# Performance work log

Hardware: AMD Instinct MI355X
Metric: run time of the kernel (lower is better)

Reference implementation:

```python
import jax, jax.numpy as jnp
import numpy as np

M, N, K, D_IN, BATCH = 800, 8, 25, 784, 256
MN = M * N


def _uniform(key, shape, fan_in):
    bound = 1.0 / np.sqrt(fan_in)
    return jax.random.uniform(key, shape, jnp.float32, -bound, bound)


def setup_inputs() -> dict:
    key = jax.random.key(0)
    ks = jax.random.split(key, 7)
    return {
        "batch_x": jax.random.normal(ks[0], (BATCH, D_IN), jnp.float32),
        "W_a": _uniform(ks[1], (M, D_IN), D_IN),   # linear_a: D_in -> m
        "b_a": _uniform(ks[2], (M,), D_IN),
        "W_b": _uniform(ks[3], (MN, MN), MN),      # linear_b: mn -> mn (dominant GEMV)
        "b_b": _uniform(ks[4], (MN,), MN),
        "W_d": _uniform(ks[5], (D_IN, M), M),      # linear_d: m -> D_in
        "b_d": _uniform(ks[6], (D_IN,), M),
    }


def reference(batch_x, W_a, b_a, W_b, b_b, W_d, b_d):
    def step(carry, x):
        x_b, phi = carry
        a = W_a @ x + b_a                                   # (M,)
        # torch: linear_a(x).repeat(1, n) -> TILED layout [g0..g_{M-1}] * N
        sigma = jnp.tile(a, N) + W_b @ x_b + b_b            # (MN,)
        pi = (1.0 - phi) * (sigma - sigma.min() + 1.0)      # (MN,)
        # torch topk(pi, 1, dim=1) on shape (1, MN): single GLOBAL argmax one-hot
        m_pi = jnp.zeros(MN, sigma.dtype).at[jnp.argmax(pi)].set(1.0)
        lam = pi.reshape(M, N).max(axis=1)                  # group max, (M,)
        _, idx = jax.lax.top_k(lam, K)
        m_lam = jnp.zeros(M, sigma.dtype).at[idx].set(1.0)  # k winning groups
        y = jnp.tanh(m_pi * jnp.tile(m_lam, N) * sigma)     # (MN,)
        x_a_pred = W_d @ y.reshape(M, N).max(axis=1) + b_d  # (D_IN,)
        # torch takes max against zero buffers self.phi/self.psi -> max(0, y)
        phi_new = jnp.maximum(0.0, y)
        psi_new = jnp.maximum(0.0, y)
        alpha = psi_new.sum()
        alpha = jnp.where(alpha == 0, jnp.asarray(1.0, alpha.dtype), alpha)
        x_b_new = jax.lax.stop_gradient(psi_new / alpha)
        return (x_b_new, phi_new), (x_a_pred, psi_new)

    init = (jnp.zeros(MN, batch_x.dtype), jnp.zeros(MN, batch_x.dtype))
    (x_b, phi), (preds, psis) = jax.lax.scan(step, init, batch_x)
    return preds, x_b, phi, psis[-1]
```

## Files before the change

kernel.cpp:

```cpp
#include <hip/hip_runtime.h>
#include <math.h>

#define MM     800
#define NN     8
#define KSEL   25
#define DIN    784
#define TSTEPS 256
#define MN     6400
#define SCTH   512
#define NWAVE  8
#define REM    288

#define NEGINF __int_as_float(0xff800000)

typedef float vf4 __attribute__((ext_vector_type(4)));

#define LDS_BARRIER() asm volatile("s_waitcnt lgkmcnt(0)\n\ts_barrier" ::: "memory")

#define WRED_STAGE(ctrl, rm)                                                   \
  {                                                                            \
    const float _ov = __int_as_float(__builtin_amdgcn_update_dpp(              \
        (int)0xFF7FFFFF, __float_as_int(bv), ctrl, rm, 0xF, false));           \
    const int _oi = __builtin_amdgcn_update_dpp(MN, bi, ctrl, rm, 0xF, false); \
    const float _om = __int_as_float(__builtin_amdgcn_update_dpp(              \
        0x7F7FFFFF, __float_as_int(lmin), ctrl, rm, 0xF, false));              \
    lmin = fminf(lmin, _om);                                                   \
    if (_ov > bv || (_ov == bv && _oi < bi)) { bv = _ov; bi = _oi; }           \
  }

#define SEL2(vA, iA, vB, iB)                                                   \
  if ((vB) > (vA)) { (vA) = (vB); (iA) = (iB); }

#define CMB(va, ia, vb, ib)                                                    \
  if ((vb) > (va) || ((vb) == (va) && (ib) < (ia))) { (va) = (vb); (ia) = (ib); }

__global__ __launch_bounds__(256) void gemm_a_kernel(
    const float* __restrict__ x,
    const float* __restrict__ Wa,
    const float* __restrict__ ba,
    float* __restrict__ A)
{
  __shared__ float4 sx4[DIN / 4];
  const int t = blockIdx.x;
  const int tid = threadIdx.x;
  if (tid < DIN / 4) sx4[tid] = ((const float4*)(x + t * DIN))[tid];
  __syncthreads();
  const int lane = tid & 63, wid = tid >> 6;
  for (int m = wid; m < MM; m += 4) {
    const float4* wrow = (const float4*)(Wa + m * DIN);
    float p = 0.f;
    for (int k4 = lane; k4 < DIN / 4; k4 += 64) {
      float4 w = wrow[k4];
      float4 xv = sx4[k4];
      p += w.x * xv.x + w.y * xv.y + w.z * xv.z + w.w * xv.w;
    }
    for (int off = 32; off; off >>= 1) p += __shfl_down(p, off, 64);
    if (lane == 0) A[t * MM + m] = p + ba[m];
  }
}

__global__ __launch_bounds__(256) void transpose_wd(
    const float* __restrict__ Wd, float* __restrict__ WdT)
{
  __shared__ float tile[32][33];
  const int bx = blockIdx.x * 32;
  const int by = blockIdx.y * 32;
  const int tx = threadIdx.x, ty = threadIdx.y;
  for (int r = ty; r < 32; r += 8) {
    int d = by + r, g = bx + tx;
    if (d < DIN && g < MM) tile[r][tx] = Wd[d * MM + g];
  }
  __syncthreads();
  for (int r = ty; r < 32; r += 8) {
    int g = bx + r, d = by + tx;
    if (g < MM && d < DIN) WdT[g * DIN + d] = tile[tx][r];
  }
}

__global__ __launch_bounds__(256) void transpose_wb64(
    const float* __restrict__ Wb, float* __restrict__ WbT)
{
  __shared__ float tile[64][65];
  const int bx = blockIdx.x * 64;
  const int by = blockIdx.y * 64;
  const int tx = threadIdx.x & 15;
  const int ty = threadIdx.x >> 4;
#pragma unroll
  for (int r = 0; r < 64; r += 16) {
    vf4 v = __builtin_nontemporal_load(
        (const vf4*)(Wb + (size_t)(by + r + ty) * MN + bx + 4 * tx));
    tile[r + ty][4 * tx + 0] = v[0];
    tile[r + ty][4 * tx + 1] = v[1];
    tile[r + ty][4 * tx + 2] = v[2];
    tile[r + ty][4 * tx + 3] = v[3];
  }
  __syncthreads();
#pragma unroll
  for (int r = 0; r < 64; r += 16) {
    float4 v;
    v.x = tile[4 * tx + 0][r + ty];
    v.y = tile[4 * tx + 1][r + ty];
    v.z = tile[4 * tx + 2][r + ty];
    v.w = tile[4 * tx + 3][r + ty];
    *(float4*)(WbT + (size_t)(bx + r + ty) * MN + by + 4 * tx) = v;
  }
}

__global__ __launch_bounds__(SCTH) void scan_kernel(
    const float* __restrict__ Wb,
    const float* __restrict__ WbT,
    const float* __restrict__ bb,
    const float* __restrict__ bd,
    const float* __restrict__ Wd,
    const float* __restrict__ WdT,
    const float* __restrict__ A,
    float* __restrict__ out)
{
  __shared__ float s_lam[2][MM];
  __shared__ __align__(16) float s_pmin[2][NWAVE];
  __shared__ __align__(16) float s_pbv[2][NWAVE];
  __shared__ __align__(16) int   s_pbi[2][NWAVE];
  __shared__ __align__(8)  float s_jpi[2][2];

  const int tid = threadIdx.x;
  const int lane = tid & 63, wid = tid >> 6;
  const bool has2 = (tid < REM);
  const int g0 = tid, g1 = tid + SCTH;

  int aoff[2];
  float4 bbv[2][2], av[2][2], cv[2][2];
#pragma unroll
  for (int s = 0; s < 2; s++) {
    const int g = tid + SCTH * s;
    const bool v = (s == 0) || has2;
    aoff[s] = 2 * (g % 100);
    if (v) {
      bbv[s][0] = ((const float4*)bb)[2 * g];
      bbv[s][1] = ((const float4*)bb)[2 * g + 1];
      av[s][0] = ((const float4*)A)[aoff[s]];
      av[s][1] = ((const float4*)A)[aoff[s] + 1];
    } else {
      bbv[s][0] = bbv[s][1] = make_float4(0.f, 0.f, 0.f, 0.f);
      av[s][0] = av[s][1] = make_float4(0.f, 0.f, 0.f, 0.f);
    }
    cv[s][0] = cv[s][1] = make_float4(0.f, 0.f, 0.f, 0.f);
  }
  float4 bd4 = make_float4(0.f, 0.f, 0.f, 0.f);
  if (tid < DIN / 4) bd4 = ((const float4*)bd)[tid];

  int jp = -1;
  float phiv = 0.f;
  int act = 0;

  for (int t = 0; t < TSTEPS; t++) {
    const int p = t & 1;
    const int jpg = jp >> 3;
    const int kxe = jp & 7;

    float4 an[2][2];
#pragma unroll
    for (int s = 0; s < 2; s++) an[s][0] = an[s][1] = make_float4(0.f, 0.f, 0.f, 0.f);
    if (t + 1 < TSTEPS) {
      const float4* ar = (const float4*)(A + (size_t)(t + 1) * MM);
#pragma unroll
      for (int s = 0; s < 2; s++) {
        const bool v = (s == 0) || has2;
        if (v) { an[s][0] = ar[aoff[s]]; an[s][1] = ar[aoff[s] + 1]; }
      }
    }

    float e0[8], e1[8];
    if (act) {
      e0[0] = (av[0][0].x + cv[0][0].x) + bbv[0][0].x;
      e0[1] = (av[0][0].y + cv[0][0].y) + bbv[0][0].y;
      e0[2] = (av[0][0].z + cv[0][0].z) + bbv[0][0].z;
      e0[3] = (av[0][0].w + cv[0][0].w) + bbv[0][0].w;
      e0[4] = (av[0][1].x + cv[0][1].x) + bbv[0][1].x;
      e0[5] = (av[0][1].y + cv[0][1].y) + bbv[0][1].y;
      e0[6] = (av[0][1].z + cv[0][1].z) + bbv[0][1].z;
      e0[7] = (av[0][1].w + cv[0][1].w) + bbv[0][1].w;
      e1[0] = (av[1][0].x + cv[1][0].x) + bbv[1][0].x;
      e1[1] = (av[1][0].y + cv[1][0].y) + bbv[1][0].y;
      e1[2] = (av[1][0].z + cv[1][0].z) + bbv[1][0].z;
      e1[3] = (av[1][0].w + cv[1][0].w) + bbv[1][0].w;
      e1[4] = (av[1][1].x + cv[1][1].x) + bbv[1][1].x;
      e1[5] = (av[1][1].y + cv[1][1].y) + bbv[1][1].y;
      e1[6] = (av[1][1].z + cv[1][1].z) + bbv[1][1].z;
      e1[7] = (av[1][1].w + cv[1][1].w) + bbv[1][1].w;
    } else {
      e0[0] = av[0][0].x + bbv[0][0].x;  e0[1] = av[0][0].y + bbv[0][0].y;
      e0[2] = av[0][0].z + bbv[0][0].z;  e0[3] = av[0][0].w + bbv[0][0].w;
      e0[4] = av[0][1].x + bbv[0][1].x;  e0[5] = av[0][1].y + bbv[0][1].y;
      e0[6] = av[0][1].z + bbv[0][1].z;  e0[7] = av[0][1].w + bbv[0][1].w;
      e1[0] = av[1][0].x + bbv[1][0].x;  e1[1] = av[1][0].y + bbv[1][0].y;
      e1[2] = av[1][0].z + bbv[1][0].z;  e1[3] = av[1][0].w + bbv[1][0].w;
      e1[4] = av[1][1].x + bbv[1][1].x;  e1[5] = av[1][1].y + bbv[1][1].y;
      e1[6] = av[1][1].z + bbv[1][1].z;  e1[7] = av[1][1].w + bbv[1][1].w;
    }

    const int kx0 = (jpg == g0) ? kxe : 8;
    const int kx1 = (has2 && jpg == g1) ? kxe : 8;
    float w0 = (kx0 == 0) ? NEGINF : e0[0];  int x0 = 8 * g0 + 0;
    float w1 = (kx0 == 1) ? NEGINF : e0[1];  int x1 = 8 * g0 + 1;
    float w2 = (kx0 == 2) ? NEGINF : e0[2];  int x2 = 8 * g0 + 2;
    float w3 = (kx0 == 3) ? NEGINF : e0[3];  int x3 = 8 * g0 + 3;
    float w4 = (kx0 == 4) ? NEGINF : e0[4];  int x4 = 8 * g0 + 4;
    float w5 = (kx0 == 5) ? NEGINF : e0[5];  int x5 = 8 * g0 + 5;
    float w6 = (kx0 == 6) ? NEGINF : e0[6];  int x6 = 8 * g0 + 6;
    float w7 = (kx0 == 7) ? NEGINF : e0[7];  int x7 = 8 * g0 + 7;
    SEL2(w0, x0, w1, x1); SEL2(w2, x2, w3, x3);
    SEL2(w4, x4, w5, x5); SEL2(w6, x6, w7, x7);
    SEL2(w0, x0, w2, x2); SEL2(w4, x4, w6, x6);
    SEL2(w0, x0, w4, x4);
    const float mxg0 = w0;
    float y0 = (has2 && kx1 != 0) ? e1[0] : NEGINF;  int z0 = has2 ? 8 * g1 + 0 : MN;
    float y1 = (has2 && kx1 != 1) ? e1[1] : NEGINF;  int z1 = has2 ? 8 * g1 + 1 : MN;
    float y2 = (has2 && kx1 != 2) ? e1[2] : NEGINF;  int z2 = has2 ? 8 * g1 + 2 : MN;
    float y3 = (has2 && kx1 != 3) ? e1[3] : NEGINF;  int z3 = has2 ? 8 * g1 + 3 : MN;
    float y4 = (has2 && kx1 != 4) ? e1[4] : NEGINF;  int z4 = has2 ? 8 * g1 + 4 : MN;
    float y5 = (has2 && kx1 != 5) ? e1[5] : NEGINF;  int z5 = has2 ? 8 * g1 + 5 : MN;
    float y6 = (has2 && kx1 != 6) ? e1[6] : NEGINF;  int z6 = has2 ? 8 * g1 + 6 : MN;
    float y7 = (has2 && kx1 != 7) ? e1[7] : NEGINF;  int z7 = has2 ? 8 * g1 + 7 : MN;
    SEL2(y0, z0, y1, z1); SEL2(y2, z2, y3, z3);
    SEL2(y4, z4, y5, z5); SEL2(y6, z6, y7, z7);
    SEL2(y0, z0, y2, z2); SEL2(y4, z4, y6, z6);
    SEL2(y0, z0, y4, z4);
    const float mxg1 = y0;
    float bv = w0; int bi = x0;
    SEL2(bv, bi, y0, z0);

    float gm0, gm1;
    {
      float a = fmaxf(e0[0], e0[1]), b = fmaxf(e0[2], e0[3]);
      float c = fmaxf(e0[4], e0[5]), d = fmaxf(e0[6], e0[7]);
      gm0 = fmaxf(fmaxf(a, b), fmaxf(c, d));
      a = fmaxf(e1[0], e1[1]); b = fmaxf(e1[2], e1[3]);
      c = fmaxf(e1[4], e1[5]); d = fmaxf(e1[6], e1[7]);
      gm1 = fmaxf(fmaxf(a, b), fmaxf(c, d));
    }
    float lmin;
    {
      float a = fminf(e0[0], e0[1]), b = fminf(e0[2], e0[3]);
      float c = fminf(e0[4], e0[5]), d = fminf(e0[6], e0[7]);
      float m0 = fminf(fminf(a, b), fminf(c, d));
      a = fminf(e1[0], e1[1]); b = fminf(e1[2], e1[3]);
      c = fminf(e1[4], e1[5]); d = fminf(e1[6], e1[7]);
      float m1 = fminf(fminf(a, b), fminf(c, d));
      lmin = has2 ? fminf(m0, m1) : m0;
    }
    s_lam[p][g0] = gm0;
    if (has2) s_lam[p][g1] = gm1;

    if (jpg == g0 || (has2 && jpg == g1)) {
      const bool own0 = (jpg == g0);
      float sjp = own0 ? e0[0] : e1[0];
#pragma unroll
      for (int k = 1; k < 8; k++) {
        const float cand = own0 ? e0[k] : e1[k];
        sjp = (kxe == k) ? cand : sjp;
      }
      s_jpi[p][0] = own0 ? mxg0 : mxg1;
      s_jpi[p][1] = sjp;
    }

    WRED_STAGE(0x111, 0xF);
    WRED_STAGE(0x112, 0xF);
    WRED_STAGE(0x114, 0xF);
    WRED_STAGE(0x118, 0xF);
    WRED_STAGE(0x142, 0xa);
    WRED_STAGE(0x143, 0xc);
    if (lane == 63) {
      s_pmin[p][wid] = lmin;
      s_pbv[p][wid] = bv;
      s_pbi[p][wid] = bi;
    }

    LDS_BARRIER();

    const float4 qa = ((const float4*)&s_pmin[p][0])[0];
    const float4 qb = ((const float4*)&s_pmin[p][0])[1];
    const float4 ra = ((const float4*)&s_pbv[p][0])[0];
    const float4 rb = ((const float4*)&s_pbv[p][0])[1];
    const int4  ua = ((const int4*)&s_pbi[p][0])[0];
    const int4  ub = ((const int4*)&s_pbi[p][0])[1];
    const float2 jpi = *(const float2*)&s_jpi[p][0];

    float smin, sigj;
    int jstar;
    {
      const float mn = fminf(fminf(fminf(qa.x, qa.y), fminf(qa.z, qa.w)),
                             fminf(fminf(qb.x, qb.y), fminf(qb.z, qb.w)));
      float V0 = ra.x, V1 = ra.y, V2 = ra.z, V3 = ra.w;
      float V4 = rb.x, V5 = rb.y, V6 = rb.z, V7 = rb.w;
      int I0 = ua.x, I1 = ua.y, I2 = ua.z, I3 = ua.w;
      int I4 = ub.x, I5 = ub.y, I6 = ub.z, I7 = ub.w;
      CMB(V0, I0, V1, I1); CMB(V2, I2, V3, I3);
      CMB(V4, I4, V5, I5); CMB(V6, I6, V7, I7);
      CMB(V0, I0, V2, I2); CMB(V4, I4, V6, I6);
      CMB(V0, I0, V4, I4);
      int js = I0;
      float sv = V0;
      if (jp >= 0) {
        const float sjp = jpi.y;
        const float piA = V0 - mn + 1.f;
        const float pip = (sjp - mn + 1.f) * (1.f - phiv);
        if (pip > piA || (pip == piA && jp < I0)) { js = jp; sv = sjp; }
      }
      smin = mn;
      jstar = js;
      sigj = sv;
    }
    const int jsr = __builtin_amdgcn_readfirstlane(jstar);
    const int gw = jsr >> 3;
    const int q = jsr % MM;

    float4 wd4 = make_float4(0.f, 0.f, 0.f, 0.f);
    if (tid < DIN / 4) {
      if (WdT) {
        wd4 = ((const float4*)(WdT + (size_t)gw * DIN))[tid];
      } else {
        wd4.x = Wd[(size_t)(4 * tid + 0) * MM + gw];
        wd4.y = Wd[(size_t)(4 * tid + 1) * MM + gw];
        wd4.z = Wd[(size_t)(4 * tid + 2) * MM + gw];
        wd4.w = Wd[(size_t)(4 * tid + 3) * MM + gw];
      }
    }

    if (t + 1 < TSTEPS) {
      if (WbT) {
        const float4* w4 = (const float4*)(WbT + (size_t)jsr * MN);
#pragma unroll
        for (int s = 0; s < 2; s++) {
          const bool v = (s == 0) || has2;
          const int g = tid + SCTH * s;
          if (v) { cv[s][0] = w4[2 * g]; cv[s][1] = w4[2 * g + 1]; }
        }
      } else {
#pragma unroll
        for (int s = 0; s < 2; s++) {
          const bool v = (s == 0) || has2;
          const int g = tid + SCTH * s;
          if (v) {
            const int jb = 8 * g;
            cv[s][0].x = Wb[(size_t)(jb + 0) * MN + jsr];
            cv[s][0].y = Wb[(size_t)(jb + 1) * MN + jsr];
            cv[s][0].z = Wb[(size_t)(jb + 2) * MN + jsr];
            cv[s][0].w = Wb[(size_t)(jb + 3) * MN + jsr];
            cv[s][1].x = Wb[(size_t)(jb + 4) * MN + jsr];
            cv[s][1].y = Wb[(size_t)(jb + 5) * MN + jsr];
            cv[s][1].z = Wb[(size_t)(jb + 6) * MN + jsr];
            cv[s][1].w = Wb[(size_t)(jb + 7) * MN + jsr];
          }
        }
      }
    }

    __builtin_amdgcn_sched_barrier(0);

    const float4* lam4 = (const float4*)&s_lam[p][0];
    float4 kv0 = lam4[lane];
    float4 kv1 = lam4[lane + 64];
    float4 kv2 = lam4[lane + 128];
    float4 kv3 = make_float4(-3.4e38f, -3.4e38f, -3.4e38f, -3.4e38f);
    if (lane < 8) kv3 = lam4[lane + 192];

    float lamfix = -3.4e38f;
    if (jp >= 0) {
      const float mxg = jpi.x;
      const float sjp = jpi.y;
      lamfix = fmaxf(mxg - smin + 1.f, (sjp - smin + 1.f) * (1.f - phiv));
    }
    const float keyq = (q == jpg) ? lamfix : (s_lam[p][q] - smin + 1.f);

    int cnt = 0;
    {
      const float kk[16] = {kv0.x, kv0.y, kv0.z, kv0.w, kv1.x, kv1.y, kv1.z, kv1.w,
                            kv2.x, kv2.y, kv2.z, kv2.w, kv3.x, kv3.y, kv3.z, kv3.w};
#pragma unroll
      for (int i = 0; i < 4; i++) {
        const bool vld = (i < 3) || (lane < 8);
#pragma unroll
        for (int c = 0; c < 4; c++) {
          const int gb = 4 * (lane + 64 * i) + c;
          const float key = (gb == jpg) ? lamfix : (kk[4 * i + c] - smin + 1.f);
          if (vld && (key > keyq || (key == keyq && gb < q))) cnt++;
        }
      }
      cnt += __builtin_amdgcn_update_dpp(0, cnt, 0x111, 0xF, 0xF, false);
      cnt += __builtin_amdgcn_update_dpp(0, cnt, 0x112, 0xF, 0xF, false);
      cnt += __builtin_amdgcn_update_dpp(0, cnt, 0x114, 0xF, 0xF, false);
      cnt += __builtin_amdgcn_update_dpp(0, cnt, 0x118, 0xF, 0xF, false);
      cnt += __builtin_amdgcn_update_dpp(0, cnt, 0x142, 0xa, 0xF, false);
      cnt += __builtin_amdgcn_update_dpp(0, cnt, 0x143, 0xc, 0xF, false);
    }
    const int total = __builtin_amdgcn_readlane(cnt, 63);

    const int inK = (total < KSEL) ? 1 : 0;
    const int nact = (inK && sigj > 0.f) ? 1 : 0;
    const float ts = tanhf(sigj);
    const float ypos = inK ? fmaxf(ts, 0.f) : 0.f;

    if (tid < DIN / 4) {
      float4 pr;
      pr.x = wd4.x * ypos + bd4.x;
      pr.y = wd4.y * ypos + bd4.y;
      pr.z = wd4.z * ypos + bd4.z;
      pr.w = wd4.w * ypos + bd4.w;
      *(float4*)(out + (size_t)t * DIN + 4 * tid) = pr;
    }
    if (t == TSTEPS - 1) {
      const float xbv = nact ? 1.f : 0.f;
      float* tail = out + TSTEPS * DIN;
      for (int idx = tid; idx < 3 * MN; idx += SCTH) {
        float vwr = 0.f;
        if (idx == jsr)               vwr = xbv;
        else if (idx == MN + jsr)     vwr = ypos;
        else if (idx == 2 * MN + jsr) vwr = ypos;
        tail[idx] = vwr;
      }
    }

    jp = jsr;
    phiv = ypos;
    act = nact;
    if (t + 1 < TSTEPS) {
#pragma unroll
      for (int s = 0; s < 2; s++) { av[s][0] = an[s][0]; av[s][1] = an[s][1]; }
    }
  }
}

extern "C" void kernel_launch(void* const* d_in, const int* in_sizes, int n_in,
                              void* d_out, int out_size, void* d_ws, size_t ws_size,
                              hipStream_t stream) {
  const float* x  = (const float*)d_in[0];
  const float* Wa = (const float*)d_in[1];
  const float* ba = (const float*)d_in[2];
  const float* Wb = (const float*)d_in[3];
  const float* bb = (const float*)d_in[4];
  const float* Wd = (const float*)d_in[5];
  const float* bd = (const float*)d_in[6];
  float* out = (float*)d_out;

  const size_t A_FLOATS   = (size_t)TSTEPS * MM;
  const size_t WDT_FLOATS = (size_t)MM * DIN;
  const size_t WBT_FLOATS = (size_t)MN * MN;

  float* Aptr;
  float* WdTptr = nullptr;
  float* WbTptr = nullptr;
  if (ws_size >= (WBT_FLOATS + WDT_FLOATS + A_FLOATS) * sizeof(float)) {
    WbTptr = (float*)d_ws;
    WdTptr = WbTptr + WBT_FLOATS;
    Aptr   = WdTptr + WDT_FLOATS;
  } else if (ws_size >= (WDT_FLOATS + A_FLOATS) * sizeof(float)) {
    WdTptr = (float*)d_ws;
    Aptr   = WdTptr + WDT_FLOATS;
  } else if (ws_size >= A_FLOATS * sizeof(float)) {
    Aptr = (float*)d_ws;
  } else {
    Aptr = out;
  }

  hipLaunchKernelGGL(gemm_a_kernel, dim3(TSTEPS), dim3(256), 0, stream,
                     x, Wa, ba, Aptr);
  if (WdTptr) {
    hipLaunchKernelGGL(transpose_wd, dim3(25, 25), dim3(32, 8), 0, stream,
                       Wd, WdTptr);
  }
  if (WbTptr) {
    hipLaunchKernelGGL(transpose_wb64, dim3(100, 100), dim3(256), 0, stream,
                       Wb, WbTptr);
  }
  hipLaunchKernelGGL(scan_kernel, dim3(1), dim3(SCTH), 0, stream,
                     Wb, WbTptr, bb, bd, Wd, WdTptr, Aptr, out);
}
```

Baseline: 1.471 ms.

## Fuse prep kernels and scan into one launch with flag-based overlap

Merges the Wa GEMM, the Wd and Wb transposes and the sequential scan into a single persistent kernel. Producer blocks set per-chunk release flags, and the scan block polls them so it can start before all preprocessing finishes. Until a band is ready the scan falls back to strided loads from the untransposed weights. The GEMM is also batched over four timesteps per block. The cost is a memset plus polling overhead, and correctness depends on the scan block running at the same time as the producer blocks.

```diff
diff --git a/kernel.cpp b/kernel.cpp
--- a/kernel.cpp
+++ b/kernel.cpp
@@ -13,7 +13,20 @@
 
 #define NEGINF __int_as_float(0xff800000)
 
+#define NB_WBBAND 100
+#define NB_GEMM4  64
+#define NB_WDBAND 25
+#define NB_MEGA   (NB_WBBAND + NB_GEMM4 + NB_WDBAND + 1)
+
+#define FLG_WB    0
+#define FLG_WBCNT 100
+#define FLG_WD    104
+#define FLG_A     132
+#define FLG_BYTES 1024
+
 typedef float vf4 __attribute__((ext_vector_type(4)));
+typedef unsigned int u32;
+typedef unsigned long long u64;
 
 #define LDS_BARRIER() asm volatile("s_waitcnt lgkmcnt(0)\n\ts_barrier" ::: "memory")
 
@@ -34,79 +47,19 @@
 #define CMB(va, ia, vb, ib)                                                    \
   if ((vb) > (va) || ((vb) == (va) && (ib) < (ia))) { (va) = (vb); (ia) = (ib); }
 
-__global__ __launch_bounds__(256) void gemm_a_kernel(
-    const float* __restrict__ x,
-    const float* __restrict__ Wa,
-    const float* __restrict__ ba,
-    float* __restrict__ A)
-{
-  __shared__ float4 sx4[DIN / 4];
-  const int t = blockIdx.x;
-  const int tid = threadIdx.x;
-  if (tid < DIN / 4) sx4[tid] = ((const float4*)(x + t * DIN))[tid];
-  __syncthreads();
-  const int lane = tid & 63, wid = tid >> 6;
-  for (int m = wid; m < MM; m += 4) {
-    const float4* wrow = (const float4*)(Wa + m * DIN);
-    float p = 0.f;
-    for (int k4 = lane; k4 < DIN / 4; k4 += 64) {
-      float4 w = wrow[k4];
-      float4 xv = sx4[k4];
-      p += w.x * xv.x + w.y * xv.y + w.z * xv.z + w.w * xv.w;
-    }
-    for (int off = 32; off; off >>= 1) p += __shfl_down(p, off, 64);
-    if (lane == 0) A[t * MM + m] = p + ba[m];
-  }
-}
-
-__global__ __launch_bounds__(256) void transpose_wd(
-    const float* __restrict__ Wd, float* __restrict__ WdT)
-{
-  __shared__ float tile[32][33];
-  const int bx = blockIdx.x * 32;
-  const int by = blockIdx.y * 32;
-  const int tx = threadIdx.x, ty = threadIdx.y;
-  for (int r = ty; r < 32; r += 8) {
-    int d = by + r, g = bx + tx;
-    if (d < DIN && g < MM) tile[r][tx] = Wd[d * MM + g];
-  }
-  __syncthreads();
-  for (int r = ty; r < 32; r += 8) {
-    int g = bx + r, d = by + tx;
-    if (g < MM && d < DIN) WdT[g * DIN + d] = tile[tx][r];
-  }
-}
-
-__global__ __launch_bounds__(256) void transpose_wb64(
-    const float* __restrict__ Wb, float* __restrict__ WbT)
-{
-  __shared__ float tile[64][65];
-  const int bx = blockIdx.x * 64;
-  const int by = blockIdx.y * 64;
-  const int tx = threadIdx.x & 15;
-  const int ty = threadIdx.x >> 4;
-#pragma unroll
-  for (int r = 0; r < 64; r += 16) {
-    vf4 v = __builtin_nontemporal_load(
-        (const vf4*)(Wb + (size_t)(by + r + ty) * MN + bx + 4 * tx));
-    tile[r + ty][4 * tx + 0] = v[0];
-    tile[r + ty][4 * tx + 1] = v[1];
-    tile[r + ty][4 * tx + 2] = v[2];
-    tile[r + ty][4 * tx + 3] = v[3];
-  }
-  __syncthreads();
-#pragma unroll
-  for (int r = 0; r < 64; r += 16) {
-    float4 v;
-    v.x = tile[4 * tx + 0][r + ty];
-    v.y = tile[4 * tx + 1][r + ty];
-    v.z = tile[4 * tx + 2][r + ty];
-    v.w = tile[4 * tx + 3][r + ty];
-    *(float4*)(WbT + (size_t)(bx + r + ty) * MN + by + 4 * tx) = v;
-  }
-}
-
-__global__ __launch_bounds__(SCTH) void scan_kernel(
+__device__ __forceinline__ u32 flag_acq(const u32* p) {
+  return __hip_atomic_load(p, __ATOMIC_ACQUIRE, __HIP_MEMORY_SCOPE_AGENT);
+}
+__device__ __forceinline__ void flag_wait(const u32* p) {
+  while (flag_acq(p) == 0u) __builtin_amdgcn_s_sleep(2);
+}
+__device__ __forceinline__ void flag_release(u32* p) {
+  __threadfence();
+  __hip_atomic_store(p, 1u, __ATOMIC_RELEASE, __HIP_MEMORY_SCOPE_AGENT);
+}
+
+template <bool POLL>
+__device__ __forceinline__ void scan_body(
     const float* __restrict__ Wb,
     const float* __restrict__ WbT,
     const float* __restrict__ bb,
@@ -114,7 +67,8 @@
     const float* __restrict__ Wd,
     const float* __restrict__ WdT,
     const float* __restrict__ A,
-    float* __restrict__ out)
+    float* __restrict__ out,
+    u32* __restrict__ flg)
 {
   __shared__ float s_lam[2][MM];
   __shared__ __align__(16) float s_pmin[2][NWAVE];
@@ -126,6 +80,13 @@
   const int lane = tid & 63, wid = tid >> 6;
   const bool has2 = (tid < REM);
   const int g0 = tid, g1 = tid + SCTH;
+
+  int a_seen = 0;
+  u32 wd_seen = 0;
+  u64 wb_seen0 = 0, wb_seen1 = 0;
+  bool wb_all = false;
+
+  if (POLL) flag_wait(&flg[FLG_A + 0]);
 
   int aoff[2];
   float4 bbv[2][2], av[2][2], cv[2][2];
@@ -161,6 +122,10 @@
 #pragma unroll
     for (int s = 0; s < 2; s++) an[s][0] = an[s][1] = make_float4(0.f, 0.f, 0.f, 0.f);
     if (t + 1 < TSTEPS) {
+      if (POLL) {
+        const int c = (t + 1) >> 2;
+        if (c >= a_seen) { flag_wait(&flg[FLG_A + c]); a_seen = c + 1; }
+      }
       const float4* ar = (const float4*)(A + (size_t)(t + 1) * MM);
 #pragma unroll
       for (int s = 0; s < 2; s++) {
@@ -316,7 +281,16 @@
 
     float4 wd4 = make_float4(0.f, 0.f, 0.f, 0.f);
     if (tid < DIN / 4) {
-      if (WdT) {
+      bool fastD = (WdT != nullptr);
+      if (POLL && fastD) {
+        const int wdb = gw >> 5;
+        const u32 bit = 1u << wdb;
+        if (!(wd_seen & bit)) {
+          if (flag_acq(&flg[FLG_WD + wdb]) != 0u) wd_seen |= bit;
+          else fastD = false;
+        }
+      }
+      if (fastD) {
         wd4 = ((const float4*)(WdT + (size_t)gw * DIN))[tid];
       } else {
         wd4.x = Wd[(size_t)(4 * tid + 0) * MM + gw];
@@ -327,7 +301,18 @@
     }
 
     if (t + 1 < TSTEPS) {
-      if (WbT) {
+      bool fastT = (WbT != nullptr);
+      if (POLL && fastT && !wb_all) {
+        const int wbb = jsr >> 6;
+        const bool have = (wbb < 64) ? (((wb_seen0 >> wbb) & 1ull) != 0)
+                                     : (((wb_seen1 >> (wbb - 64)) & 1ull) != 0);
+        if (!have) {
+          if (flag_acq(&flg[FLG_WB + wbb]) != 0u) {
+            if (wbb < 64) wb_seen0 |= 1ull << wbb; else wb_seen1 |= 1ull << (wbb - 64);
+          } else fastT = false;
+        }
+      }
+      if (fastT) {
         const float4* w4 = (const float4*)(WbT + (size_t)jsr * MN);
 #pragma unroll
         for (int s = 0; s < 2; s++) {
@@ -364,6 +349,10 @@
     float4 kv3 = make_float4(-3.4e38f, -3.4e38f, -3.4e38f, -3.4e38f);
     if (lane < 8) kv3 = lam4[lane + 192];
 
+    if (POLL && !wb_all) {
+      if (flag_acq(&flg[FLG_WBCNT]) == (u32)NB_WBBAND) wb_all = true;
+    }
+
     float lamfix = -3.4e38f;
     if (jp >= 0) {
       const float mxg = jpi.x;
@@ -428,6 +417,169 @@
       for (int s = 0; s < 2; s++) { av[s][0] = an[s][0]; av[s][1] = an[s][1]; }
     }
   }
+  (void)flg;
+}
+
+__global__ __launch_bounds__(512) void mega_kernel(
+    const float* __restrict__ x, const float* __restrict__ Wa,
+    const float* __restrict__ ba, float* __restrict__ A,
+    const float* __restrict__ Wd, float* __restrict__ WdT,
+    const float* __restrict__ Wb, float* __restrict__ WbT,
+    const float* __restrict__ bb, const float* __restrict__ bd,
+    float* __restrict__ out, u32* __restrict__ flg)
+{
+  __shared__ __align__(16) float smem[64 * 65];
+  const int bid = blockIdx.x;
+  const int tid = threadIdx.x;
+
+  if (bid < NB_WBBAND) {
+    const int bx = bid * 64;
+    const int tx = tid & 15;
+    const int ty = tid >> 4;
+    for (int st = 0; st < 100; ++st) {
+      const int by = st * 64;
+#pragma unroll
+      for (int r = 0; r < 64; r += 32) {
+        vf4 v = __builtin_nontemporal_load(
+            (const vf4*)(Wb + (size_t)(by + r + ty) * MN + bx + 4 * tx));
+        smem[(r + ty) * 65 + 4 * tx + 0] = v[0];
+        smem[(r + ty) * 65 + 4 * tx + 1] = v[1];
+        smem[(r + ty) * 65 + 4 * tx + 2] = v[2];
+        smem[(r + ty) * 65 + 4 * tx + 3] = v[3];
+      }
+      __syncthreads();
+#pragma unroll
+      for (int r = 0; r < 64; r += 32) {
+        float4 v;
+        v.x = smem[(4 * tx + 0) * 65 + r + ty];
+        v.y = smem[(4 * tx + 1) * 65 + r + ty];
+        v.z = smem[(4 * tx + 2) * 65 + r + ty];
+        v.w = smem[(4 * tx + 3) * 65 + r + ty];
+        *(float4*)(WbT + (size_t)(bx + r + ty) * MN + by + 4 * tx) = v;
+      }
+      __syncthreads();
+    }
+    if (tid == 0) {
+      flag_release(&flg[FLG_WB + bid]);
+      __hip_atomic_fetch_add(&flg[FLG_WBCNT], 1u, __ATOMIC_ACQ_REL,
+                             __HIP_MEMORY_SCOPE_AGENT);
+    }
+    return;
+  }
+
+  if (bid < NB_WBBAND + NB_GEMM4) {
+    const int b = bid - NB_WBBAND;
+    const int t0 = b * 4;
+    float4* sx = (float4*)smem;
+    for (int i = tid; i < 4 * (DIN / 4); i += 512)
+      sx[i] = ((const float4*)(x + (size_t)(t0 + i / 196) * DIN))[i % 196];
+    __syncthreads();
+    const int lane = tid & 63, wid = tid >> 6;
+    for (int m = wid; m < MM; m += 8) {
+      const float4* wrow = (const float4*)(Wa + (size_t)m * DIN);
+      float p0 = 0.f, p1 = 0.f, p2 = 0.f, p3 = 0.f;
+      for (int k4 = lane; k4 < DIN / 4; k4 += 64) {
+        float4 w = wrow[k4];
+        float4 a0 = sx[k4];
+        float4 a1 = sx[196 + k4];
+        float4 a2 = sx[392 + k4];
+        float4 a3 = sx[588 + k4];
+        p0 += w.x * a0.x + w.y * a0.y + w.z * a0.z + w.w * a0.w;
+        p1 += w.x * a1.x + w.y * a1.y + w.z * a1.z + w.w * a1.w;
+        p2 += w.x * a2.x + w.y * a2.y + w.z * a2.z + w.w * a2.w;
+        p3 += w.x * a3.x + w.y * a3.y + w.z * a3.z + w.w * a3.w;
+      }
+      for (int off = 32; off; off >>= 1) {
+        p0 += __shfl_down(p0, off, 64);
+        p1 += __shfl_down(p1, off, 64);
+        p2 += __shfl_down(p2, off, 64);
+        p3 += __shfl_down(p3, off, 64);
+      }
+      if (lane == 0) {
+        const float bv = ba[m];
+        A[(size_t)(t0 + 0) * MM + m] = p0 + bv;
+        A[(size_t)(t0 + 1) * MM + m] = p1 + bv;
+        A[(size_t)(t0 + 2) * MM + m] = p2 + bv;
+        A[(size_t)(t0 + 3) * MM + m] = p3 + bv;
+      }
+    }
+    __syncthreads();
+    if (tid == 0) flag_release(&flg[FLG_A + b]);
+    return;
+  }
+
+  if (bid < NB_WBBAND + NB_GEMM4 + NB_WDBAND) {
+    const int b = bid - NB_WBBAND - NB_GEMM4;
+    const int bx = b * 32;
+    const int tx = tid & 31, ty = tid >> 5;
+    for (int dt = 0; dt < 25; ++dt) {
+      const int by = dt * 32;
+      for (int r = ty; r < 32; r += 16) {
+        int d = by + r, g = bx + tx;
+        if (d < DIN && g < MM) smem[r * 33 + tx] = Wd[(size_t)d * MM + g];
+      }
+      __syncthreads();
+      for (int r = ty; r < 32; r += 16) {
+        int g = bx + r, d = by + tx;
+        if (g < MM && d < DIN) WdT[(size_t)g * DIN + d] = smem[tx * 33 + r];
+      }
+      __syncthreads();
+    }
+    if (tid == 0) flag_release(&flg[FLG_WD + b]);
+    return;
+  }
+
+  scan_body<true>(Wb, WbT, bb, bd, Wd, WdT, A, out, flg);
+}
+
+__global__ __launch_bounds__(256) void gemm_a_kernel(
+    const float* __restrict__ x, const float* __restrict__ Wa,
+    const float* __restrict__ ba, float* __restrict__ A)
+{
+  __shared__ float4 sx4[DIN / 4];
+  const int t = blockIdx.x;
+  const int tid = threadIdx.x;
+  if (tid < DIN / 4) sx4[tid] = ((const float4*)(x + t * DIN))[tid];
+  __syncthreads();
+  const int lane = tid & 63, wid = tid >> 6;
+  for (int m = wid; m < MM; m += 4) {
+    const float4* wrow = (const float4*)(Wa + m * DIN);
+    float p = 0.f;
+    for (int k4 = lane; k4 < DIN / 4; k4 += 64) {
+      float4 w = wrow[k4];
+      float4 xv = sx4[k4];
+      p += w.x * xv.x + w.y * xv.y + w.z * xv.z + w.w * xv.w;
+    }
+    for (int off = 32; off; off >>= 1) p += __shfl_down(p, off, 64);
+    if (lane == 0) A[t * MM + m] = p + ba[m];
+  }
+}
+
+__global__ __launch_bounds__(256) void transpose_wd(
+    const float* __restrict__ Wd, float* __restrict__ WdT)
+{
+  __shared__ float tile[32][33];
+  const int bx = blockIdx.x * 32;
+  const int by = blockIdx.y * 32;
+  const int tx = threadIdx.x, ty = threadIdx.y;
+  for (int r = ty; r < 32; r += 8) {
+    int d = by + r, g = bx + tx;
+    if (d < DIN && g < MM) tile[r][tx] = Wd[d * MM + g];
+  }
+  __syncthreads();
+  for (int r = ty; r < 32; r += 8) {
+    int g = bx + r, d = by + tx;
+    if (g < MM && d < DIN) WdT[g * DIN + d] = tile[tx][r];
+  }
+}
+
+__global__ __launch_bounds__(SCTH) void scan_kernel_serial(
+    const float* __restrict__ Wb, const float* __restrict__ WbT,
+    const float* __restrict__ bb, const float* __restrict__ bd,
+    const float* __restrict__ Wd, const float* __restrict__ WdT,
+    const float* __restrict__ A, float* __restrict__ out)
+{
+  scan_body<false>(Wb, WbT, bb, bd, Wd, WdT, A, out, nullptr);
 }
 
 extern "C" void kernel_launch(void* const* d_in, const int* in_sizes, int n_in,
@@ -445,15 +597,29 @@
   const size_t A_FLOATS   = (size_t)TSTEPS * MM;
   const size_t WDT_FLOATS = (size_t)MM * DIN;
   const size_t WBT_FLOATS = (size_t)MN * MN;
+  const size_t BASE_BYTES = (WBT_FLOATS + WDT_FLOATS) * sizeof(float);
+
+  if (ws_size >= BASE_BYTES + FLG_BYTES) {
+    float* WbTptr = (float*)d_ws;
+    float* WdTptr = WbTptr + WBT_FLOATS;
+    float* Aptr;
+    u32* flg;
+    if (ws_size >= BASE_BYTES + A_FLOATS * sizeof(float) + FLG_BYTES) {
+      Aptr = WdTptr + WDT_FLOATS;
+      flg = (u32*)(Aptr + A_FLOATS);
+    } else {
+      Aptr = out;
+      flg = (u32*)(WdTptr + WDT_FLOATS);
+    }
+    hipMemsetAsync(flg, 0, FLG_BYTES, stream);
+    hipLaunchKernelGGL(mega_kernel, dim3(NB_MEGA), dim3(512), 0, stream,
+                       x, Wa, ba, Aptr, Wd, WdTptr, Wb, WbTptr, bb, bd, out, flg);
+    return;
+  }
 
   float* Aptr;
   float* WdTptr = nullptr;
-  float* WbTptr = nullptr;
-  if (ws_size >= (WBT_FLOATS + WDT_FLOATS + A_FLOATS) * sizeof(float)) {
-    WbTptr = (float*)d_ws;
-    WdTptr = WbTptr + WBT_FLOATS;
-    Aptr   = WdTptr + WDT_FLOATS;
-  } else if (ws_size >= (WDT_FLOATS + A_FLOATS) * sizeof(float)) {
+  if (ws_size >= (WDT_FLOATS + A_FLOATS) * sizeof(float)) {
     WdTptr = (float*)d_ws;
     Aptr   = WdTptr + WDT_FLOATS;
   } else if (ws_size >= A_FLOATS * sizeof(float)) {
@@ -461,17 +627,12 @@
   } else {
     Aptr = out;
   }
-
   hipLaunchKernelGGL(gemm_a_kernel, dim3(TSTEPS), dim3(256), 0, stream,
                      x, Wa, ba, Aptr);
   if (WdTptr) {
     hipLaunchKernelGGL(transpose_wd, dim3(25, 25), dim3(32, 8), 0, stream,
                        Wd, WdTptr);
   }
-  if (WbTptr) {
-    hipLaunchKernelGGL(transpose_wb64, dim3(100, 100), dim3(256), 0, stream,
-                       Wb, WbTptr);
-  }
-  hipLaunchKernelGGL(scan_kernel, dim3(1), dim3(SCTH), 0, stream,
-                     Wb, WbTptr, bb, bd, Wd, WdTptr, Aptr, out);
-}
+  hipLaunchKernelGGL(scan_kernel_serial, dim3(1), dim3(SCTH), 0, stream,
+                     Wb, nullptr, bb, bd, Wd, WdTptr, Aptr, out);
+}
```

New measurement: 1.435 ms. 1.02x faster.
